# Performance work log

Measured on AMD Instinct MI355X. Metric: run time of the kernel, lower is better.

## Reference

```python
import jax, jax.numpy as jnp
import numpy as np

D, H, Wd, V, OUTF = 256, 512, 512, 32, 256


def setup_inputs() -> dict:
    key = jax.random.key(0)
    k1, k2, k3, k4 = jax.random.split(key, 4)
    X = jax.random.normal(k1, (1, D, H, Wd), dtype=jnp.float32)
    W = jax.random.normal(k2, (D, V), dtype=jnp.float32)
    # variance is divided by; keep it bounded away from zero
    variance = jax.random.uniform(k3, (D, V), dtype=jnp.float32, minval=0.5, maxval=1.5)
    weight = jax.random.normal(k4, (D, OUTF), dtype=jnp.float32) * 0.05
    return {"X": X, "W": W, "variance": variance, "weight": weight}


def reference(X, W, variance, weight):
    _, d, h, w = X.shape
    outf = weight.shape[1]
    # torch does reshape(X, (h, w, d)) -> flatten to (h*w, d); plain reshape, faithful
    Xf = jnp.reshape(X, (h * w, d))
    iv = 1.0 / variance          # (d, V)
    iv2 = iv * iv
    # Q[p,i] = sum_d ((x_pd - W_di) / var_di)^2, expanded into 2 GEMMs + bias
    Q = (Xf * Xf) @ iv2 - 2.0 * (Xf @ (W * iv2)) + jnp.sum(W * W * iv2, axis=0)[None, :]
    Q = Q - jnp.min(Q, axis=1, keepdims=True)
    Q = jnp.exp(-0.5 * Q)
    Q = Q / jnp.sum(Q, axis=1, keepdims=True)      # (hw, V) row-stochastic
    s = jnp.sum(Q, axis=0)                          # (V,)
    # Z[:,i] = sum_p Q_pi * (x_p - W[:,i]) / var[:,i] / s_i
    Z = ((Xf.T @ Q) - W * s[None, :]) * iv / s[None, :]   # (d, V)
    # original divides by sum of squares (not its sqrt) -- keep faithful
    Z = Z / jnp.sum(Z * Z, axis=0, keepdims=True)
    Adj = Z.T @ Z                                   # (V, V)
    Zo = jax.nn.relu(Adj @ (Z.T @ weight))          # (V, outf)
    Xn = Q @ Zo                                     # (hw, outf)
    # torch: reshape (h, w, outf) then .view(1, outf, h, w) == plain reshape
    return jnp.reshape(Xn, (1, outf, h, w))
```

## Files before the change

### kernel.cpp

```cpp
#include <hip/hip_runtime.h>

#define D_    256
#define V_    32
#define HW_   (512*512)
#define OUTF_ 256

__global__ __launch_bounds__(256) void k1_q(const float* __restrict__ X,
                                            const float* __restrict__ W,
                                            const float* __restrict__ var,
                                            float* __restrict__ Q,
                                            float* __restrict__ s_out)
{
    __shared__ float As[D_][V_];
    __shared__ float Bs[D_][V_];
    const int tid = threadIdx.x;

    {
        const float* wr = W   + tid * V_;
        const float* vr = var + tid * V_;
        #pragma unroll
        for (int i = 0; i < V_; ++i) {
            float iv = 1.0f / vr[i];
            As[tid][i] = wr[i] * iv;
            Bs[tid][i] = iv;
        }
    }
    __syncthreads();

    const size_t pA = (size_t)blockIdx.x * 512 + tid;
    const size_t pB = pA + 256;
    const float4* xrowA = (const float4*)(X + pA * D_);
    const float4* xrowB = (const float4*)(X + pB * D_);

    float tA[V_], tB[V_];
    #pragma unroll
    for (int i = 0; i < V_; ++i) { tA[i] = 0.f; tB[i] = 0.f; }

    for (int d4 = 0; d4 < D_/4; ++d4) {
        float4 xa = xrowA[d4];
        float4 xb = xrowB[d4];
        float xsa[4] = {xa.x, xa.y, xa.z, xa.w};
        float xsb[4] = {xb.x, xb.y, xb.z, xb.w};
        #pragma unroll
        for (int k = 0; k < 4; ++k) {
            const int d = d4*4 + k;
            const float xA = xsa[k];
            const float xB = xsb[k];
            #pragma unroll
            for (int i = 0; i < V_; ++i) {
                const float bi = Bs[d][i];
                const float ai = As[d][i];
                float eA = fmaf(xA, bi, -ai);
                float eB = fmaf(xB, bi, -ai);
                tA[i] = fmaf(eA, eA, tA[i]);
                tB[i] = fmaf(eB, eB, tB[i]);
            }
        }
    }

    float qA[V_], qB[V_];
    float mnA = 3.4e38f, mnB = 3.4e38f;
    #pragma unroll
    for (int i = 0; i < V_; ++i) { mnA = fminf(mnA, tA[i]); mnB = fminf(mnB, tB[i]); }
    float sumA = 0.f, sumB = 0.f;
    #pragma unroll
    for (int i = 0; i < V_; ++i) {
        qA[i] = __expf(-0.5f * (tA[i] - mnA));  sumA += qA[i];
        qB[i] = __expf(-0.5f * (tB[i] - mnB));  sumB += qB[i];
    }
    const float invA = 1.0f / sumA;
    const float invB = 1.0f / sumB;

    float4* qoutA = (float4*)(Q + pA * V_);
    float4* qoutB = (float4*)(Q + pB * V_);
    #pragma unroll
    for (int j = 0; j < V_/4; ++j) {
        float4 oa, ob;
        oa.x = qA[4*j+0]*invA; oa.y = qA[4*j+1]*invA; oa.z = qA[4*j+2]*invA; oa.w = qA[4*j+3]*invA;
        ob.x = qB[4*j+0]*invB; ob.y = qB[4*j+1]*invB; ob.z = qB[4*j+2]*invB; ob.w = qB[4*j+3]*invB;
        qoutA[j] = oa;
        qoutB[j] = ob;
    }

    __syncthreads();
    float* s_blk = &As[0][0];
    if (tid < V_) s_blk[tid] = 0.f;
    __syncthreads();
    #pragma unroll
    for (int i = 0; i < V_; ++i) {
        atomicAdd(&s_blk[i], qA[i]*invA + qB[i]*invB);
    }
    __syncthreads();
    if (tid < V_) atomicAdd(&s_out[tid], s_blk[tid]);
}

__global__ __launch_bounds__(256) void k2_m(const float* __restrict__ X,
                                            const float* __restrict__ Q,
                                            float* __restrict__ M)
{
    const int d = threadIdx.x;
    const size_t p0 = (size_t)blockIdx.x * 512;
    float acc[V_];
    #pragma unroll
    for (int i = 0; i < V_; ++i) acc[i] = 0.f;

    for (int pp = 0; pp < 512; ++pp) {
        const size_t p = p0 + pp;
        const float x = X[p * D_ + d];
        const float* qr = Q + p * V_;
        #pragma unroll
        for (int i = 0; i < V_; ++i) acc[i] = fmaf(x, qr[i], acc[i]);
    }
    #pragma unroll
    for (int i = 0; i < V_; ++i) atomicAdd(&M[d*V_ + i], acc[i]);
}

__global__ __launch_bounds__(256) void k3a(const float* __restrict__ M,
                                           const float* __restrict__ s_in,
                                           const float* __restrict__ W,
                                           const float* __restrict__ var,
                                           float* __restrict__ Z,
                                           float* __restrict__ Adj)
{
    __shared__ float Zl[D_][V_];
    __shared__ float ss[V_];
    __shared__ float nrm[V_];
    const int t = threadIdx.x;
    if (t < V_) ss[t] = s_in[t];
    __syncthreads();

    #pragma unroll
    for (int i = 0; i < V_; ++i) {
        float iv = 1.0f / var[t*V_ + i];
        float z = (M[t*V_ + i] - W[t*V_ + i] * ss[i]) * iv / ss[i];
        Zl[t][i] = z;
    }
    __syncthreads();
    if (t < V_) {
        float n = 0.f;
        for (int d = 0; d < D_; ++d) { float z = Zl[d][t]; n = fmaf(z, z, n); }
        nrm[t] = n;
    }
    __syncthreads();
    #pragma unroll
    for (int i = 0; i < V_; ++i) {
        float z = Zl[t][i] / nrm[i];
        Zl[t][i] = z;
        Z[t*V_ + i] = z;
    }
    __syncthreads();
    #pragma unroll
    for (int e = 0; e < 4; ++e) {
        int idx = t*4 + e;
        int i = idx >> 5, j = idx & 31;
        float a = 0.f;
        for (int d = 0; d < D_; ++d) a = fmaf(Zl[d][i], Zl[d][j], a);
        Adj[idx] = a;
    }
}

__global__ __launch_bounds__(256) void k3b(const float* __restrict__ Z,
                                           const float* __restrict__ weight,
                                           const float* __restrict__ Adj,
                                           float* __restrict__ Zo)
{
    __shared__ float T[V_];
    const int t = threadIdx.x;
    const int f = blockIdx.x;
    if (t < V_) T[t] = 0.f;
    __syncthreads();
    const float wt = weight[t*OUTF_ + f];
    const float* zr = Z + t*V_;
    #pragma unroll
    for (int j = 0; j < V_; ++j) atomicAdd(&T[j], zr[j] * wt);
    __syncthreads();
    if (t < V_) {
        float o = 0.f;
        #pragma unroll
        for (int j = 0; j < V_; ++j) o = fmaf(Adj[t*V_ + j], T[j], o);
        Zo[t*OUTF_ + f] = fmaxf(o, 0.f);
    }
}

__global__ __launch_bounds__(256) void k4_out(const float* __restrict__ Q,
                                              const float* __restrict__ Zo,
                                              float* __restrict__ out)
{
    __shared__ float Qt[256][V_];
    const int t = threadIdx.x;
    const size_t p0 = (size_t)blockIdx.x * 256;

    float zc[V_];
    #pragma unroll
    for (int i = 0; i < V_; ++i) zc[i] = Zo[i*OUTF_ + t];

    {
        float4* dst = (float4*)(&Qt[t][0]);
        const float4* src = (const float4*)(Q + (p0 + t) * V_);
        #pragma unroll
        for (int j = 0; j < V_/4; ++j) dst[j] = src[j];
    }
    __syncthreads();

    #pragma unroll 2
    for (int p = 0; p < 256; ++p) {
        float a0 = 0.f, a1 = 0.f, a2 = 0.f, a3 = 0.f;
        #pragma unroll
        for (int i = 0; i < V_; i += 4) {
            a0 = fmaf(Qt[p][i+0], zc[i+0], a0);
            a1 = fmaf(Qt[p][i+1], zc[i+1], a1);
            a2 = fmaf(Qt[p][i+2], zc[i+2], a2);
            a3 = fmaf(Qt[p][i+3], zc[i+3], a3);
        }
        out[(p0 + p) * OUTF_ + t] = (a0 + a1) + (a2 + a3);
    }
}

extern "C" void kernel_launch(void* const* d_in, const int* in_sizes, int n_in,
                              void* d_out, int out_size, void* d_ws, size_t ws_size,
                              hipStream_t stream)
{
    const float* X      = (const float*)d_in[0];
    const float* W      = (const float*)d_in[1];
    const float* var    = (const float*)d_in[2];
    const float* weight = (const float*)d_in[3];
    float* out = (float*)d_out;
    float* ws  = (float*)d_ws;

    float* Q   = ws;
    float* s   = Q   + (size_t)HW_ * V_;
    float* M   = s   + V_;
    float* Z   = M   + D_ * V_;
    float* Adj = Z   + D_ * V_;
    float* Zo  = Adj + V_ * V_;

    hipMemsetAsync(s, 0, (V_ + D_*V_) * sizeof(float), stream);

    k1_q <<<HW_/512, 256, 0, stream>>>(X, W, var, Q, s);
    k2_m <<<HW_/512, 256, 0, stream>>>(X, Q, M);
    k3a  <<<1,       256, 0, stream>>>(M, s, W, var, Z, Adj);
    k3b  <<<OUTF_,   256, 0, stream>>>(Z, weight, Adj, Zo);
    k4_out<<<HW_/256, 256, 0, stream>>>(Q, Zo, out);
}
```

Measured before the change: 1.150 ms.

## Register-tile Q, M and output kernels and move column sums into M kernel

```diff
diff --git a/kernel.cpp b/kernel.cpp
--- a/kernel.cpp
+++ b/kernel.cpp
@@ -5,114 +5,156 @@
 #define HW_   (512*512)
 #define OUTF_ 256
 
-__global__ __launch_bounds__(256) void k1_q(const float* __restrict__ X,
-                                            const float* __restrict__ W,
-                                            const float* __restrict__ var,
-                                            float* __restrict__ Q,
-                                            float* __restrict__ s_out)
-{
-    __shared__ float As[D_][V_];
-    __shared__ float Bs[D_][V_];
-    const int tid = threadIdx.x;
-
-    {
-        const float* wr = W   + tid * V_;
-        const float* vr = var + tid * V_;
+__global__ __launch_bounds__(128, 1) void k1_q(const float* __restrict__ X,
+                                               const float* __restrict__ W,
+                                               const float* __restrict__ var,
+                                               float* __restrict__ Q)
+{
+    __shared__ float4 As4[D_][8];
+    __shared__ float4 Bs4[D_][8];
+    const int t = threadIdx.x;
+
+    for (int r = t; r < D_; r += 128) {
+        const float4* wr = (const float4*)(W   + r * V_);
+        const float4* vr = (const float4*)(var + r * V_);
+        #pragma unroll
+        for (int i4 = 0; i4 < 8; ++i4) {
+            float4 wv = wr[i4], vv = vr[i4];
+            float4 iv;
+            iv.x = 1.0f / vv.x; iv.y = 1.0f / vv.y;
+            iv.z = 1.0f / vv.z; iv.w = 1.0f / vv.w;
+            float4 a;
+            a.x = wv.x * iv.x; a.y = wv.y * iv.y;
+            a.z = wv.z * iv.z; a.w = wv.w * iv.w;
+            As4[r][i4] = a;
+            Bs4[r][i4] = iv;
+        }
+    }
+    __syncthreads();
+
+    const size_t pbase = (size_t)blockIdx.x * 512 + t;
+    const float* xp = X + pbase * D_;
+
+    float acc[4][V_];
+    #pragma unroll
+    for (int j = 0; j < 4; ++j)
+        #pragma unroll
+        for (int i = 0; i < V_; ++i) acc[j][i] = 0.f;
+
+    #pragma unroll 2
+    for (int d4 = 0; d4 < D_/4; ++d4) {
+        float4 xv[4];
+        #pragma unroll
+        for (int j = 0; j < 4; ++j)
+            xv[j] = *(const float4*)(xp + (size_t)j * 128 * D_ + d4 * 4);
+        #pragma unroll
+        for (int k = 0; k < 4; ++k) {
+            const int d = d4 * 4 + k;
+            #pragma unroll
+            for (int i4 = 0; i4 < 8; ++i4) {
+                const float4 a4 = As4[d][i4];
+                const float4 b4 = Bs4[d][i4];
+                #pragma unroll
+                for (int j = 0; j < 4; ++j) {
+                    const float xk = (k == 0) ? xv[j].x : (k == 1) ? xv[j].y
+                                   : (k == 2) ? xv[j].z : xv[j].w;
+                    float e0 = fmaf(xk, b4.x, -a4.x);
+                    float e1 = fmaf(xk, b4.y, -a4.y);
+                    float e2 = fmaf(xk, b4.z, -a4.z);
+                    float e3 = fmaf(xk, b4.w, -a4.w);
+                    acc[j][i4*4+0] = fmaf(e0, e0, acc[j][i4*4+0]);
+                    acc[j][i4*4+1] = fmaf(e1, e1, acc[j][i4*4+1]);
+                    acc[j][i4*4+2] = fmaf(e2, e2, acc[j][i4*4+2]);
+                    acc[j][i4*4+3] = fmaf(e3, e3, acc[j][i4*4+3]);
+                }
+            }
+        }
+    }
+
+    #pragma unroll
+    for (int j = 0; j < 4; ++j) {
+        float mn = 3.4e38f;
+        #pragma unroll
+        for (int i = 0; i < V_; ++i) mn = fminf(mn, acc[j][i]);
+        float sum = 0.f;
         #pragma unroll
         for (int i = 0; i < V_; ++i) {
-            float iv = 1.0f / vr[i];
-            As[tid][i] = wr[i] * iv;
-            Bs[tid][i] = iv;
-        }
-    }
-    __syncthreads();
-
-    const size_t pA = (size_t)blockIdx.x * 512 + tid;
-    const size_t pB = pA + 256;
-    const float4* xrowA = (const float4*)(X + pA * D_);
-    const float4* xrowB = (const float4*)(X + pB * D_);
-
-    float tA[V_], tB[V_];
-    #pragma unroll
-    for (int i = 0; i < V_; ++i) { tA[i] = 0.f; tB[i] = 0.f; }
-
-    for (int d4 = 0; d4 < D_/4; ++d4) {
-        float4 xa = xrowA[d4];
-        float4 xb = xrowB[d4];
-        float xsa[4] = {xa.x, xa.y, xa.z, xa.w};
-        float xsb[4] = {xb.x, xb.y, xb.z, xb.w};
-        #pragma unroll
-        for (int k = 0; k < 4; ++k) {
-            const int d = d4*4 + k;
-            const float xA = xsa[k];
-            const float xB = xsb[k];
+            float q = __expf(-0.5f * (acc[j][i] - mn));
+            acc[j][i] = q;
+            sum += q;
+        }
+        const float inv = 1.0f / sum;
+        float* qout = Q + (pbase + (size_t)j * 128) * V_;
+        #pragma unroll
+        for (int i4 = 0; i4 < 8; ++i4) {
+            float4 o;
+            o.x = acc[j][i4*4+0] * inv; o.y = acc[j][i4*4+1] * inv;
+            o.z = acc[j][i4*4+2] * inv; o.w = acc[j][i4*4+3] * inv;
+            *(float4*)(qout + i4 * 4) = o;
+        }
+    }
+}
+
+__global__ __launch_bounds__(64, 2) void k2_m(const float* __restrict__ X,
+                                              const float* __restrict__ Q,
+                                              float* __restrict__ M,
+                                              float* __restrict__ s_out)
+{
+    __shared__ float4 Qs[64][8];
+    const int t = threadIdx.x;
+    const size_t p0 = (size_t)blockIdx.x * 128;
+
+    float acc[4][V_];
+    #pragma unroll
+    for (int k = 0; k < 4; ++k)
+        #pragma unroll
+        for (int i = 0; i < V_; ++i) acc[k][i] = 0.f;
+
+    float sacc = 0.f;
+    const int si = t & 31, sh = t >> 5;
+
+    for (int ch = 0; ch < 2; ++ch) {
+        const size_t pc = p0 + ch * 64;
+        const float4* qsrc = (const float4*)(Q + pc * V_);
+        #pragma unroll
+        for (int j = 0; j < 8; ++j) {
+            int L = j * 64 + t;
+            Qs[L >> 3][L & 7] = qsrc[L];
+        }
+        __syncthreads();
+
+        #pragma unroll 4
+        for (int pp = 0; pp < 32; ++pp)
+            sacc += ((const float*)&Qs[sh * 32 + pp][0])[si];
+
+        #pragma unroll 2
+        for (int pp = 0; pp < 64; ++pp) {
+            const float4 x4 = *(const float4*)(X + (pc + pp) * D_ + 4 * t);
             #pragma unroll
-            for (int i = 0; i < V_; ++i) {
-                const float bi = Bs[d][i];
-                const float ai = As[d][i];
-                float eA = fmaf(xA, bi, -ai);
-                float eB = fmaf(xB, bi, -ai);
-                tA[i] = fmaf(eA, eA, tA[i]);
-                tB[i] = fmaf(eB, eB, tB[i]);
+            for (int i4 = 0; i4 < 8; ++i4) {
+                const float4 q4 = Qs[pp][i4];
+                #pragma unroll
+                for (int c = 0; c < 4; ++c) {
+                    const float qv = (c == 0) ? q4.x : (c == 1) ? q4.y
+                                   : (c == 2) ? q4.z : q4.w;
+                    acc[0][i4*4+c] = fmaf(x4.x, qv, acc[0][i4*4+c]);
+                    acc[1][i4*4+c] = fmaf(x4.y, qv, acc[1][i4*4+c]);
+                    acc[2][i4*4+c] = fmaf(x4.z, qv, acc[2][i4*4+c]);
+                    acc[3][i4*4+c] = fmaf(x4.w, qv, acc[3][i4*4+c]);
+                }
             }
         }
-    }
-
-    float qA[V_], qB[V_];
-    float mnA = 3.4e38f, mnB = 3.4e38f;
-    #pragma unroll
-    for (int i = 0; i < V_; ++i) { mnA = fminf(mnA, tA[i]); mnB = fminf(mnB, tB[i]); }
-    float sumA = 0.f, sumB = 0.f;
-    #pragma unroll
-    for (int i = 0; i < V_; ++i) {
-        qA[i] = __expf(-0.5f * (tA[i] - mnA));  sumA += qA[i];
-        qB[i] = __expf(-0.5f * (tB[i] - mnB));  sumB += qB[i];
-    }
-    const float invA = 1.0f / sumA;
-    const float invB = 1.0f / sumB;
-
-    float4* qoutA = (float4*)(Q + pA * V_);
-    float4* qoutB = (float4*)(Q + pB * V_);
-    #pragma unroll
-    for (int j = 0; j < V_/4; ++j) {
-        float4 oa, ob;
-        oa.x = qA[4*j+0]*invA; oa.y = qA[4*j+1]*invA; oa.z = qA[4*j+2]*invA; oa.w = qA[4*j+3]*invA;
-        ob.x = qB[4*j+0]*invB; ob.y = qB[4*j+1]*invB; ob.z = qB[4*j+2]*invB; ob.w = qB[4*j+3]*invB;
-        qoutA[j] = oa;
-        qoutB[j] = ob;
-    }
-
-    __syncthreads();
-    float* s_blk = &As[0][0];
-    if (tid < V_) s_blk[tid] = 0.f;
-    __syncthreads();
-    #pragma unroll
-    for (int i = 0; i < V_; ++i) {
-        atomicAdd(&s_blk[i], qA[i]*invA + qB[i]*invB);
-    }
-    __syncthreads();
-    if (tid < V_) atomicAdd(&s_out[tid], s_blk[tid]);
-}
-
-__global__ __launch_bounds__(256) void k2_m(const float* __restrict__ X,
-                                            const float* __restrict__ Q,
-                                            float* __restrict__ M)
-{
-    const int d = threadIdx.x;
-    const size_t p0 = (size_t)blockIdx.x * 512;
-    float acc[V_];
-    #pragma unroll
-    for (int i = 0; i < V_; ++i) acc[i] = 0.f;
-
-    for (int pp = 0; pp < 512; ++pp) {
-        const size_t p = p0 + pp;
-        const float x = X[p * D_ + d];
-        const float* qr = Q + p * V_;
-        #pragma unroll
-        for (int i = 0; i < V_; ++i) acc[i] = fmaf(x, qr[i], acc[i]);
-    }
-    #pragma unroll
-    for (int i = 0; i < V_; ++i) atomicAdd(&M[d*V_ + i], acc[i]);
+        __syncthreads();
+    }
+
+    #pragma unroll
+    for (int k = 0; k < 4; ++k)
+        #pragma unroll
+        for (int i = 0; i < V_; ++i)
+            atomicAdd(&M[(4 * t + k) * V_ + i], acc[k][i]);
+
+    sacc += __shfl_down(sacc, 32);
+    if (t < V_) atomicAdd(&s_out[t], sacc);
 }
 
 __global__ __launch_bounds__(256) void k3a(const float* __restrict__ M,
@@ -132,8 +174,7 @@
     #pragma unroll
     for (int i = 0; i < V_; ++i) {
         float iv = 1.0f / var[t*V_ + i];
-        float z = (M[t*V_ + i] - W[t*V_ + i] * ss[i]) * iv / ss[i];
-        Zl[t][i] = z;
+        Zl[t][i] = (M[t*V_ + i] - W[t*V_ + i] * ss[i]) * iv / ss[i];
     }
     __syncthreads();
     if (t < V_) {
@@ -182,37 +223,47 @@
     }
 }
 
-__global__ __launch_bounds__(256) void k4_out(const float* __restrict__ Q,
-                                              const float* __restrict__ Zo,
-                                              float* __restrict__ out)
-{
-    __shared__ float Qt[256][V_];
-    const int t = threadIdx.x;
+__global__ __launch_bounds__(256, 2) void k4_out(const float* __restrict__ Q,
+                                                 const float* __restrict__ Zo,
+                                                 float* __restrict__ out)
+{
+    __shared__ float4 Qt[256][8];
+    const int t  = threadIdx.x;
+    const int fq = t & 63;
+    const int w  = t >> 6;
     const size_t p0 = (size_t)blockIdx.x * 256;
 
-    float zc[V_];
-    #pragma unroll
-    for (int i = 0; i < V_; ++i) zc[i] = Zo[i*OUTF_ + t];
-
-    {
-        float4* dst = (float4*)(&Qt[t][0]);
-        const float4* src = (const float4*)(Q + (p0 + t) * V_);
-        #pragma unroll
-        for (int j = 0; j < V_/4; ++j) dst[j] = src[j];
+    float4 zc[V_];
+    #pragma unroll
+    for (int i = 0; i < V_; ++i)
+        zc[i] = *(const float4*)(Zo + i * OUTF_ + 4 * fq);
+
+    const float4* qsrc = (const float4*)(Q + p0 * V_);
+    #pragma unroll
+    for (int j = 0; j < 8; ++j) {
+        int L = j * 256 + t;
+        Qt[L >> 3][L & 7] = qsrc[L];
     }
     __syncthreads();
 
     #pragma unroll 2
-    for (int p = 0; p < 256; ++p) {
-        float a0 = 0.f, a1 = 0.f, a2 = 0.f, a3 = 0.f;
-        #pragma unroll
-        for (int i = 0; i < V_; i += 4) {
-            a0 = fmaf(Qt[p][i+0], zc[i+0], a0);
-            a1 = fmaf(Qt[p][i+1], zc[i+1], a1);
-            a2 = fmaf(Qt[p][i+2], zc[i+2], a2);
-            a3 = fmaf(Qt[p][i+3], zc[i+3], a3);
-        }
-        out[(p0 + p) * OUTF_ + t] = (a0 + a1) + (a2 + a3);
+    for (int pp = w * 64; pp < w * 64 + 64; ++pp) {
+        float4 a; a.x = 0.f; a.y = 0.f; a.z = 0.f; a.w = 0.f;
+        #pragma unroll
+        for (int i4 = 0; i4 < 8; ++i4) {
+            const float4 q4 = Qt[pp][i4];
+            #pragma unroll
+            for (int c = 0; c < 4; ++c) {
+                const float qv = (c == 0) ? q4.x : (c == 1) ? q4.y
+                               : (c == 2) ? q4.z : q4.w;
+                const float4 z4 = zc[i4*4+c];
+                a.x = fmaf(qv, z4.x, a.x);
+                a.y = fmaf(qv, z4.y, a.y);
+                a.z = fmaf(qv, z4.z, a.z);
+                a.w = fmaf(qv, z4.w, a.w);
+            }
+        }
+        *(float4*)(out + (p0 + pp) * OUTF_ + 4 * fq) = a;
     }
 }
 
@@ -236,9 +287,9 @@
 
     hipMemsetAsync(s, 0, (V_ + D_*V_) * sizeof(float), stream);
 
-    k1_q <<<HW_/512, 256, 0, stream>>>(X, W, var, Q, s);
-    k2_m <<<HW_/512, 256, 0, stream>>>(X, Q, M);
-    k3a  <<<1,       256, 0, stream>>>(M, s, W, var, Z, Adj);
-    k3b  <<<OUTF_,   256, 0, stream>>>(Z, weight, Adj, Zo);
-    k4_out<<<HW_/256, 256, 0, stream>>>(Q, Zo, out);
-}
+    k1_q  <<<512,      128, 0, stream>>>(X, W, var, Q);
+    k2_m  <<<HW_/128,  64,  0, stream>>>(X, Q, M, s);
+    k3a   <<<1,        256, 0, stream>>>(M, s, W, var, Z, Adj);
+    k3b   <<<OUTF_,    256, 0, stream>>>(Z, weight, Adj, Zo);
+    k4_out<<<HW_/256,  256, 0, stream>>>(Q, Zo, out);
+}
```

After: 2.470 ms. +114.7%, slower.
